# Optimization experiments

Measured on AMD Instinct MI355X. Metric: run time of the kernel, lower is better.

## Reference

```python
import jax, jax.numpy as jnp
import numpy as np

N, E = 100000, 400000
IN, HID, H, D = 165, 128, 8, 16  # per-head dim D = HID // H
NUM_CLASSES = 2


def layer_norm(x, g, b, eps=1e-5):
    m = jnp.mean(x, axis=-1, keepdims=True)
    v = jnp.var(x, axis=-1, keepdims=True)
    return (x - m) / jnp.sqrt(v + eps) * g + b


def transformer_conv(x, src, dst, Wq, bq, Wk, bk, Wv, bv, Ws, bs):
    # x: [N, HID]; src/dst: [E]
    n = x.shape[0]
    q = (x @ Wq + bq).reshape(n, H, D)
    k = (x @ Wk + bk).reshape(n, H, D)
    v = (x @ Wv + bv).reshape(n, H, D)
    # per-edge attention logits: [E, H]
    alpha = jnp.sum(q[dst] * k[src], axis=-1) / jnp.sqrt(jnp.float32(D))
    # segment softmax over incoming edges of each destination node
    amax = jax.ops.segment_max(alpha, dst, num_segments=n)          # [N, H]
    amax = jnp.where(jnp.isfinite(amax), amax, 0.0)
    ex = jnp.exp(alpha - amax[dst])                                  # [E, H]
    denom = jax.ops.segment_sum(ex, dst, num_segments=n)            # [N, H]
    a = ex / (denom[dst] + 1e-16)
    msg = v[src] * a[..., None]                                      # [E, H, D]
    out = jax.ops.segment_sum(msg, dst, num_segments=n)             # [N, H, D]
    out = out.reshape(n, H * D)
    # root skip connection (root_weight=True, beta=False in PyG defaults)
    return out + x @ Ws + bs


def setup_inputs() -> dict:
    key = jax.random.key(0)
    ks = jax.random.split(key, 24)
    rn = lambda k, s: (jax.random.normal(k, s, jnp.float32) * 0.05)
    inp = {
        "x": jax.random.normal(ks[0], (N, IN), jnp.float32),
        "edge_index": jax.random.randint(ks[1], (2, E), 0, N, jnp.int32),
        "W_in": rn(ks[2], (IN, HID)), "b_in": jnp.zeros((HID,), jnp.float32),
        # layer 1 TransformerConv
        "Wq1": rn(ks[3], (HID, HID)), "bq1": jnp.zeros((HID,), jnp.float32),
        "Wk1": rn(ks[4], (HID, HID)), "bk1": jnp.zeros((HID,), jnp.float32),
        "Wv1": rn(ks[5], (HID, HID)), "bv1": jnp.zeros((HID,), jnp.float32),
        "Ws1": rn(ks[6], (HID, HID)), "bs1": jnp.zeros((HID,), jnp.float32),
        "g1": jnp.ones((HID,), jnp.float32), "be1": jnp.zeros((HID,), jnp.float32),
        # layer 2 TransformerConv
        "Wq2": rn(ks[7], (HID, HID)), "bq2": jnp.zeros((HID,), jnp.float32),
        "Wk2": rn(ks[8], (HID, HID)), "bk2": jnp.zeros((HID,), jnp.float32),
        "Wv2": rn(ks[9], (HID, HID)), "bv2": jnp.zeros((HID,), jnp.float32),
        "Ws2": rn(ks[10], (HID, HID)), "bs2": jnp.zeros((HID,), jnp.float32),
        "g2": jnp.ones((HID,), jnp.float32), "be2": jnp.zeros((HID,), jnp.float32),
        # classifier MLP
        "Wc1": rn(ks[11], (HID, HID // 2)), "bc1": jnp.zeros((HID // 2,), jnp.float32),
        "Wc2": rn(ks[12], (HID // 2, NUM_CLASSES)), "bc2": jnp.zeros((NUM_CLASSES,), jnp.float32),
    }
    return inp


def reference(x, edge_index, W_in, b_in,
              Wq1, bq1, Wk1, bk1, Wv1, bv1, Ws1, bs1, g1, be1,
              Wq2, bq2, Wk2, bk2, Wv2, bv2, Ws2, bs2, g2, be2,
              Wc1, bc1, Wc2, bc2):
    src, dst = edge_index[0], edge_index[1]
    h = x @ W_in + b_in                                   # input projection
    h_new = transformer_conv(h, src, dst, Wq1, bq1, Wk1, bk1, Wv1, bv1, Ws1, bs1)
    h = layer_norm(h + h_new, g1, be1)                    # dropout = identity (eval)
    h_new = transformer_conv(h, src, dst, Wq2, bq2, Wk2, bk2, Wv2, bv2, Ws2, bs2)
    h = layer_norm(h + h_new, g2, be2)
    return jax.nn.relu(h @ Wc1 + bc1) @ Wc2 + bc2         # [N, num_classes]
```

## Files before the change

### kernel.cpp

```cpp
#include <hip/hip_runtime.h>
#include <hip/hip_bf16.h>

#define NN 100000
#define EE 400000
#define IN_DIM 165
#define KPAD 192
#define HID 128
#define C1 64
#define NC 2
#define SCANB 256
#define NBLK 391
#define NBD2 782

typedef const float* fpp;
typedef __hip_bfloat16 bf16;
typedef __attribute__((ext_vector_type(8))) short s16x8;
typedef __attribute__((ext_vector_type(4))) float f32x4;

__device__ __forceinline__ float bflo(unsigned u) { return __uint_as_float(u << 16); }
__device__ __forceinline__ float bfhi(unsigned u) { return __uint_as_float(u & 0xFFFF0000u); }
__device__ __forceinline__ float us2f(unsigned short u) { return __uint_as_float((unsigned)u << 16); }
__device__ __forceinline__ unsigned short bfbits(float f) {
    bf16 h = __float2bfloat16(f);
    return *reinterpret_cast<unsigned short*>(&h);
}

__global__ void k_cvt_weights(fpp W_in, fpp Wq1, fpp Wk1, fpp Wv1, fpp Ws1,
                              fpp Wq2, fpp Wk2, fpp Wv2, fpp Ws2, fpp Wc1,
                              fpp bq1, fpp bk1, fpp bv1, fpp bs1,
                              fpp bq2, fpp bk2, fpp bv2, fpp bs2,
                              unsigned short* __restrict__ winpack,
                              unsigned short* __restrict__ wpack,
                              unsigned short* __restrict__ wc1t,
                              float* __restrict__ bpack) {
    int idx = blockIdx.x * blockDim.x + threadIdx.x;
    if (idx < 24576) {
        int n = idx / KPAD, k = idx % KPAD;
        float v = (k < IN_DIM) ? W_in[k * HID + n] : 0.f;
        winpack[idx] = bfbits(v);
    } else if (idx < 155648) {
        int local = idx - 24576;
        int layer = local >> 16;
        int rest = local & 65535;
        int chunk = rest >> 14;
        int l14 = rest & 16383;
        int n = l14 >> 7, k = l14 & 127;
        const float* src;
        int col;
        if (chunk == 0) { src = layer ? Wq2 : Wq1; col = n; }
        else if (chunk == 3) { src = layer ? Ws2 : Ws1; col = n; }
        else {
            int a = ((chunk == 2) ? 16 : 0) + (n >> 3), e = n & 7;
            src = (e < 4) ? (layer ? Wk2 : Wk1) : (layer ? Wv2 : Wv1);
            col = 4 * a + (e & 3);
        }
        wpack[local] = bfbits(src[k * HID + col]);
    } else if (idx < 163840) {
        int local = idx - 155648;
        int n = local >> 7, k = local & 127;
        wc1t[local] = bfbits(Wc1[k * C1 + n]);
    } else if (idx < 164864) {
        int local = idx - 163840;
        int layer = local >> 9;
        int rest = local & 511;
        int chunk = rest >> 7, n = rest & 127;
        const float* src;
        int col;
        if (chunk == 0) { src = layer ? bq2 : bq1; col = n; }
        else if (chunk == 3) { src = layer ? bs2 : bs1; col = n; }
        else {
            int a = ((chunk == 2) ? 16 : 0) + (n >> 3), e = n & 7;
            src = (e < 4) ? (layer ? bk2 : bk1) : (layer ? bv2 : bv1);
            col = 4 * a + (e & 3);
        }
        bpack[local] = src[col];
    }
}

__global__ void k_cvt_x(fpp x, unsigned short* __restrict__ xb) {
    int i = blockIdx.x * blockDim.x + threadIdx.x;
    int row = i / 24, c = i % 24;
    s16x8 us;
#pragma unroll
    for (int j = 0; j < 8; j++) {
        int col = c * 8 + j;
        float v = (col < IN_DIM) ? x[(size_t)row * IN_DIM + col] : 0.f;
        us[j] = (short)bfbits(v);
    }
    *(s16x8*)(xb + (size_t)row * KPAD + c * 8) = us;
}

__global__ void k_hist(const int* __restrict__ dst, int* __restrict__ deg) {
    int e = blockIdx.x * blockDim.x + threadIdx.x;
    if (e < EE) atomicAdd(&deg[dst[e]], 1);
}
__global__ void k_scan1(const int* __restrict__ deg, int* __restrict__ pos,
                        int* __restrict__ bsum, int n) {
    __shared__ int tmp[SCANB];
    int t = threadIdx.x, i = blockIdx.x * SCANB + t;
    int v = (i < n) ? deg[i] : 0;
    tmp[t] = v; __syncthreads();
    for (int off = 1; off < SCANB; off <<= 1) {
        int x = (t >= off) ? tmp[t - off] : 0;
        __syncthreads();
        tmp[t] += x;
        __syncthreads();
    }
    if (i < n) pos[i] = tmp[t] - v;
    if (t == SCANB - 1) bsum[blockIdx.x] = tmp[t];
}
__global__ void k_scan2(int* __restrict__ bsum, int nb) {
    __shared__ int tmp[512];
    int t = threadIdx.x;
    int v = (t < nb) ? bsum[t] : 0;
    tmp[t] = v; __syncthreads();
    for (int off = 1; off < 512; off <<= 1) {
        int x = (t >= off) ? tmp[t - off] : 0;
        __syncthreads();
        tmp[t] += x;
        __syncthreads();
    }
    if (t < nb) bsum[t] = tmp[t] - v;
}
__global__ void k_scan3(int* __restrict__ pos, const int* __restrict__ bsum,
                        const int* __restrict__ deg, int2* __restrict__ csr2, int n) {
    int i = blockIdx.x * blockDim.x + threadIdx.x;
    if (i < n) {
        int s = pos[i] + bsum[blockIdx.x];
        pos[i] = s;
        csr2[i] = make_int2(s, deg[i]);
    }
}
__global__ void k_fill(const int* __restrict__ src, const int* __restrict__ dst,
                       int* __restrict__ pos, int* __restrict__ esrc) {
    int e = blockIdx.x * blockDim.x + threadIdx.x;
    if (e < EE) {
        int p = atomicAdd(&pos[dst[e]], 1);
        esrc[p] = src[e];
    }
}

__global__ __launch_bounds__(256) void k_dense_in(const unsigned short* __restrict__ xb,
                                                  const unsigned short* __restrict__ winpack,
                                                  fpp b_in, unsigned short* __restrict__ hb) {
    __shared__ unsigned short smem[18432];
    unsigned short* As = smem;
    unsigned short* Ws = smem + 9216;
    int row0 = blockIdx.x * 128;
    int t = threadIdx.x, lane = t & 63, w = t >> 6;
    int quad = lane >> 4, l16 = lane & 15;
    int m_off = (w >> 1) * 64, n_off = (w & 1) * 64;

    f32x4 acc[4][4];
    float bias_v[4];
#pragma unroll
    for (int ni = 0; ni < 4; ni++) bias_v[ni] = b_in[n_off + ni * 16 + l16];
#pragma unroll
    for (int mi = 0; mi < 4; mi++)
#pragma unroll
        for (int ni = 0; ni < 4; ni++)
            acc[mi][ni] = (f32x4){bias_v[ni], bias_v[ni], bias_v[ni], bias_v[ni]};

    for (int kc = 0; kc < 3; kc++) {
        __syncthreads();
        for (int i = 0; i < 4; i++) {
            int g = t + i * 256;
            int r = g >> 3, c = g & 7;
            int rg = min(row0 + r, NN - 1);
            *(s16x8*)(As + r * 72 + c * 8) =
                *(const s16x8*)(xb + (size_t)rg * KPAD + kc * 64 + c * 8);
            *(s16x8*)(Ws + r * 72 + c * 8) =
                *(const s16x8*)(winpack + r * KPAD + kc * 64 + c * 8);
        }
        __syncthreads();
#pragma unroll
        for (int ks = 0; ks < 2; ks++) {
            int k0 = ks * 32;
            s16x8 a[4], b[4];
#pragma unroll
            for (int mi = 0; mi < 4; mi++)
                a[mi] = *(const s16x8*)(As + (m_off + mi * 16 + l16) * 72 + k0 + quad * 8);
#pragma unroll
            for (int ni = 0; ni < 4; ni++)
                b[ni] = *(const s16x8*)(Ws + (n_off + ni * 16 + l16) * 72 + k0 + quad * 8);
#pragma unroll
            for (int mi = 0; mi < 4; mi++)
#pragma unroll
                for (int ni = 0; ni < 4; ni++)
                    acc[mi][ni] = __builtin_amdgcn_mfma_f32_16x16x32_bf16(
                        a[mi], b[ni], acc[mi][ni], 0, 0, 0);
        }
    }
    __syncthreads();
    unsigned short* Cs = smem;
#pragma unroll
    for (int mi = 0; mi < 4; mi++)
#pragma unroll
        for (int ni = 0; ni < 4; ni++)
#pragma unroll
            for (int r = 0; r < 4; r++)
                Cs[(m_off + mi * 16 + quad * 4 + r) * 136 + n_off + ni * 16 + l16] =
                    bfbits(acc[mi][ni][r]);
    __syncthreads();
    for (int i = 0; i < 8; i++) {
        int g = t + i * 256;
        int r = g >> 4, c = g & 15;
        if (row0 + r < NN)
            *(s16x8*)(hb + (size_t)(row0 + r) * HID + c * 8) =
                *(const s16x8*)(Cs + r * 136 + c * 8);
    }
}

__global__ __launch_bounds__(256) void k_dense4(const unsigned short* __restrict__ hb,
                                                const unsigned short* __restrict__ wpackL,
                                                const float* __restrict__ bpackL,
                                                bf16* __restrict__ qb, bf16* __restrict__ kvb,
                                                bf16* __restrict__ agg) {
    __shared__ unsigned short As[128 * 136];
    __shared__ unsigned short Ws[128 * 136];
    int row0 = blockIdx.x * 128;
    int t = threadIdx.x, lane = t & 63, w = t >> 6;
    int quad = lane >> 4, l16 = lane & 15;
    int m_off = (w >> 1) * 64, n_off = (w & 1) * 64;

    for (int i = 0; i < 8; i++) {
        int g = t + i * 256;
        int r = g >> 4, c = g & 15;
        int rg = min(row0 + r, NN - 1);
        *(s16x8*)(As + r * 136 + c * 8) = *(const s16x8*)(hb + (size_t)rg * HID + c * 8);
    }
    __syncthreads();

    s16x8 afr[4][4];
#pragma unroll
    for (int ks = 0; ks < 4; ks++)
#pragma unroll
        for (int mi = 0; mi < 4; mi++)
            afr[ks][mi] = *(const s16x8*)(As + (m_off + mi * 16 + l16) * 136 + ks * 32 + quad * 8);

    for (int nc = 0; nc < 4; nc++) {
        unsigned short* tp; int stride;
        if (nc == 0)      { tp = (unsigned short*)qb;        stride = 128; }
        else if (nc == 1) { tp = (unsigned short*)kvb;       stride = 256; }
        else if (nc == 2) { tp = (unsigned short*)kvb + 128; stride = 256; }
        else              { tp = (unsigned short*)agg;       stride = 128; }
        const float* bp = bpackL + nc * 128;

        __syncthreads();
        for (int i = 0; i < 8; i++) {
            int g = t + i * 256;
            int r = g >> 4, c = g & 15;
            *(s16x8*)(Ws + r * 136 + c * 8) =
                *(const s16x8*)(wpackL + nc * 16384 + r * HID + c * 8);
        }
        __syncthreads();

        f32x4 acc[4][4];
        float bias_v[4];
#pragma unroll
        for (int ni = 0; ni < 4; ni++) bias_v[ni] = bp[n_off + ni * 16 + l16];
#pragma unroll
        for (int mi = 0; mi < 4; mi++)
#pragma unroll
            for (int ni = 0; ni < 4; ni++)
                acc[mi][ni] = (f32x4){bias_v[ni], bias_v[ni], bias_v[ni], bias_v[ni]};

#pragma unroll
        for (int ks = 0; ks < 4; ks++) {
            s16x8 b[4];
#pragma unroll
            for (int ni = 0; ni < 4; ni++)
                b[ni] = *(const s16x8*)(Ws + (n_off + ni * 16 + l16) * 136 + ks * 32 + quad * 8);
#pragma unroll
            for (int mi = 0; mi < 4; mi++)
#pragma unroll
                for (int ni = 0; ni < 4; ni++)
                    acc[mi][ni] = __builtin_amdgcn_mfma_f32_16x16x32_bf16(
                        afr[ks][mi], b[ni], acc[mi][ni], 0, 0, 0);
        }
        __syncthreads();

        unsigned short* Cs = Ws;
#pragma unroll
        for (int mi = 0; mi < 4; mi++)
#pragma unroll
            for (int ni = 0; ni < 4; ni++)
#pragma unroll
                for (int r = 0; r < 4; r++)
                    Cs[(m_off + mi * 16 + quad * 4 + r) * 136 + n_off + ni * 16 + l16] =
                        bfbits(acc[mi][ni][r]);
        __syncthreads();
        if (nc == 3) {
            for (int i = 0; i < 8; i++) {
                int g = t + i * 256;
                int r = g >> 4, c = g & 15;
                if (row0 + r < NN) {
                    s16x8 cv = *(const s16x8*)(Cs + r * 136 + c * 8);
                    s16x8 hv = *(const s16x8*)(As + r * 136 + c * 8);
                    s16x8 ov;
#pragma unroll
                    for (int j = 0; j < 8; j++)
                        ov[j] = (short)bfbits(us2f((unsigned short)cv[j]) +
                                              us2f((unsigned short)hv[j]));
                    *(s16x8*)(tp + (size_t)(row0 + r) * stride + c * 8) = ov;
                }
            }
        } else {
            for (int i = 0; i < 8; i++) {
                int g = t + i * 256;
                int r = g >> 4, c = g & 15;
                if (row0 + r < NN)
                    *(s16x8*)(tp + (size_t)(row0 + r) * stride + c * 8) =
                        *(const s16x8*)(Cs + r * 136 + c * 8);
            }
        }
    }
}

__global__ void k_agg_ln(const bf16* __restrict__ qb, const bf16* __restrict__ kvb,
                         const int2* __restrict__ csr2, const int* __restrict__ esrc,
                         const bf16* __restrict__ agg, unsigned short* __restrict__ hb,
                         fpp g, fpp b) {
    int wv = (blockIdx.x * blockDim.x + threadIdx.x) >> 6;
    int lane = threadIdx.x & 63;
    int l32 = lane & 31;
    int d = wv * 2 + (lane >> 5);
    if (d >= NN) return;
    uint2 qu = ((const uint2*)(qb + (size_t)d * HID))[l32];
    float q0 = bflo(qu.x) * 0.25f, q1 = bfhi(qu.x) * 0.25f;
    float q2 = bflo(qu.y) * 0.25f, q3 = bfhi(qu.y) * 0.25f;
    int2 se = csr2[d];
    uint2 au = ((const uint2*)(agg + (size_t)d * HID))[l32];
    float4 gv = ((const float4*)g)[l32];
    float4 bv = ((const float4*)b)[l32];
    int start = se.x, cnt = se.y;

    int sj = (l32 < cnt) ? esrc[start + l32] : 0;

    uint4 kv[8];
    float tt[8];
    float m = -INFINITY;
#pragma unroll
    for (int j = 0; j < 8; j++) {
        int s = __shfl(sj, j, 32);
        if (j < cnt) kv[j] = ((const uint4*)(kvb + (size_t)s * 256))[l32];
        else kv[j] = (uint4){0u, 0u, 0u, 0u};
        float t = q0 * bflo(kv[j].x) + q1 * bfhi(kv[j].x) +
                  q2 * bflo(kv[j].y) + q3 * bfhi(kv[j].y);
        t += __shfl_xor(t, 1);
        t += __shfl_xor(t, 2);
        tt[j] = (j < cnt) ? t : -INFINITY;
        m = fmaxf(m, tt[j]);
    }
    if (cnt == 0) m = 0.f;
    float L = 0.f, o0 = 0.f, o1 = 0.f, o2 = 0.f, o3 = 0.f;
#pragma unroll
    for (int j = 0; j < 8; j++) {
        float p = __expf(tt[j] - m);
        L += p;
        o0 += p * bflo(kv[j].z);
        o1 += p * bfhi(kv[j].z);
        o2 += p * bflo(kv[j].w);
        o3 += p * bfhi(kv[j].w);
    }

    for (int j = 8; j < min(cnt, 32); j++) {
        int s = __shfl(sj, j, 32);
        uint4 kvt = ((const uint4*)(kvb + (size_t)s * 256))[l32];
        float t = q0 * bflo(kvt.x) + q1 * bfhi(kvt.x) + q2 * bflo(kvt.y) + q3 * bfhi(kvt.y);
        t += __shfl_xor(t, 1);
        t += __shfl_xor(t, 2);
        float nm = fmaxf(m, t);
        float corr = __expf(m - nm);
        float p = __expf(t - nm);
        L = L * corr + p;
        o0 = o0 * corr + p * bflo(kvt.z);
        o1 = o1 * corr + p * bfhi(kvt.z);
        o2 = o2 * corr + p * bflo(kvt.w);
        o3 = o3 * corr + p * bfhi(kvt.w);
        m = nm;
    }
    for (int base = 32; base < cnt; base += 32) {
        int nc = min(32, cnt - base);
        int sj2 = (l32 < nc) ? esrc[start + base + l32] : 0;
        for (int j = 0; j < nc; j++) {
            int s = __shfl(sj2, j, 32);
            uint4 kvt = ((const uint4*)(kvb + (size_t)s * 256))[l32];
            float t = q0 * bflo(kvt.x) + q1 * bfhi(kvt.x) + q2 * bflo(kvt.y) + q3 * bfhi(kvt.y);
            t += __shfl_xor(t, 1);
            t += __shfl_xor(t, 2);
            float nm = fmaxf(m, t);
            float corr = __expf(m - nm);
            float p = __expf(t - nm);
            L = L * corr + p;
            o0 = o0 * corr + p * bflo(kvt.z);
            o1 = o1 * corr + p * bfhi(kvt.z);
            o2 = o2 * corr + p * bflo(kvt.w);
            o3 = o3 * corr + p * bfhi(kvt.w);
            m = nm;
        }
    }

    float inv = 1.f / (L + 1e-16f);
    float v0 = bflo(au.x) + o0 * inv;
    float v1 = bfhi(au.x) + o1 * inv;
    float v2 = bflo(au.y) + o2 * inv;
    float v3 = bfhi(au.y) + o3 * inv;
    float s = v0 + v1 + v2 + v3;
    float s2 = v0 * v0 + v1 * v1 + v2 * v2 + v3 * v3;
    for (int off = 16; off; off >>= 1) {
        s += __shfl_xor(s, off);
        s2 += __shfl_xor(s2, off);
    }
    float mn = s * (1.f / HID);
    float var = s2 * (1.f / HID) - mn * mn;
    float invs = rsqrtf(var + 1e-5f);
    float ox = (v0 - mn) * invs * gv.x + bv.x;
    float oy = (v1 - mn) * invs * gv.y + bv.y;
    float oz = (v2 - mn) * invs * gv.z + bv.z;
    float ow = (v3 - mn) * invs * gv.w + bv.w;
    uint2 outw;
    outw.x = ((unsigned)bfbits(oy) << 16) | bfbits(ox);
    outw.y = ((unsigned)bfbits(ow) << 16) | bfbits(oz);
    ((uint2*)(hb + (size_t)d * HID))[l32] = outw;
}

__global__ __launch_bounds__(256) void k_classifier(const unsigned short* __restrict__ hb,
                                                    const unsigned short* __restrict__ wc1t,
                                                    fpp bc1, fpp Wc2, fpp bc2,
                                                    float* __restrict__ out) {
    __shared__ unsigned short As[128 * 136];
    __shared__ unsigned short Ws[64 * 136];
    int row0 = blockIdx.x * 128;
    int t = threadIdx.x, lane = t & 63, w = t >> 6;
    int quad = lane >> 4, l16 = lane & 15;
    int m_off = w * 32;

    for (int i = 0; i < 8; i++) {
        int g = t + i * 256;
        int r = g >> 4, c = g & 15;
        int rg = min(row0 + r, NN - 1);
        *(s16x8*)(As + r * 136 + c * 8) = *(const s16x8*)(hb + (size_t)rg * HID + c * 8);
    }
    for (int i = 0; i < 4; i++) {
        int g = t + i * 256;
        int r = g >> 4, c = g & 15;
        *(s16x8*)(Ws + r * 136 + c * 8) = *(const s16x8*)(wc1t + r * HID + c * 8);
    }
    __syncthreads();

    f32x4 acc[2][4];
    float bias_v[4];
#pragma unroll
    for (int ni = 0; ni < 4; ni++) bias_v[ni] = bc1[ni * 16 + l16];
#pragma unroll
    for (int mi = 0; mi < 2; mi++)
#pragma unroll
        for (int ni = 0; ni < 4; ni++)
            acc[mi][ni] = (f32x4){bias_v[ni], bias_v[ni], bias_v[ni], bias_v[ni]};

#pragma unroll
    for (int ks = 0; ks < 4; ks++) {
        s16x8 a[2], b[4];
#pragma unroll
        for (int mi = 0; mi < 2; mi++)
            a[mi] = *(const s16x8*)(As + (m_off + mi * 16 + l16) * 136 + ks * 32 + quad * 8);
#pragma unroll
        for (int ni = 0; ni < 4; ni++)
            b[ni] = *(const s16x8*)(Ws + (ni * 16 + l16) * 136 + ks * 32 + quad * 8);
#pragma unroll
        for (int mi = 0; mi < 2; mi++)
#pragma unroll
            for (int ni = 0; ni < 4; ni++)
                acc[mi][ni] = __builtin_amdgcn_mfma_f32_16x16x32_bf16(
                    a[mi], b[ni], acc[mi][ni], 0, 0, 0);
    }
    __syncthreads();
    float* Cs = (float*)As;
#pragma unroll
    for (int mi = 0; mi < 2; mi++)
#pragma unroll
        for (int ni = 0; ni < 4; ni++)
#pragma unroll
            for (int r = 0; r < 4; r++)
                Cs[(m_off + mi * 16 + quad * 4 + r) * 68 + ni * 16 + l16] =
                    fmaxf(acc[mi][ni][r], 0.f);
    __syncthreads();

    int row = t >> 1, half = t & 1;
    float p0 = 0.f, p1 = 0.f;
    for (int c = half * 32; c < half * 32 + 32; c++) {
        float v = Cs[row * 68 + c];
        p0 += v * Wc2[c * NC + 0];
        p1 += v * Wc2[c * NC + 1];
    }
    p0 += __shfl_xor(p0, 1, 64);
    p1 += __shfl_xor(p1, 1, 64);
    if (half == 0 && row0 + row < NN) {
        out[(size_t)(row0 + row) * NC + 0] = p0 + bc2[0];
        out[(size_t)(row0 + row) * NC + 1] = p1 + bc2[1];
    }
}

extern "C" void kernel_launch(void* const* d_in, const int* in_sizes, int n_in,
                              void* d_out, int out_size, void* d_ws, size_t ws_size,
                              hipStream_t stream) {
    fpp x = (fpp)d_in[0];
    const int* ei = (const int*)d_in[1];
    const int* src = ei;
    const int* dst = ei + EE;
    fpp W_in = (fpp)d_in[2];  fpp b_in = (fpp)d_in[3];
    fpp Wq1 = (fpp)d_in[4];   fpp bq1 = (fpp)d_in[5];
    fpp Wk1 = (fpp)d_in[6];   fpp bk1 = (fpp)d_in[7];
    fpp Wv1 = (fpp)d_in[8];   fpp bv1 = (fpp)d_in[9];
    fpp Ws1 = (fpp)d_in[10];  fpp bs1 = (fpp)d_in[11];
    fpp g1 = (fpp)d_in[12];   fpp be1 = (fpp)d_in[13];
    fpp Wq2 = (fpp)d_in[14];  fpp bq2 = (fpp)d_in[15];
    fpp Wk2 = (fpp)d_in[16];  fpp bk2 = (fpp)d_in[17];
    fpp Wv2 = (fpp)d_in[18];  fpp bv2 = (fpp)d_in[19];
    fpp Ws2 = (fpp)d_in[20];  fpp bs2 = (fpp)d_in[21];
    fpp g2 = (fpp)d_in[22];   fpp be2 = (fpp)d_in[23];
    fpp Wc1 = (fpp)d_in[24];  fpp bc1 = (fpp)d_in[25];
    fpp Wc2 = (fpp)d_in[26];  fpp bc2 = (fpp)d_in[27];
    float* out = (float*)d_out;

    char* p = (char*)d_ws;
    unsigned short* hb = (unsigned short*)p;  p += (size_t)NN * HID * 2;
    bf16* agg = (bf16*)p;            p += (size_t)NN * HID * 2;
    bf16* qb = (bf16*)p;             p += (size_t)NN * HID * 2;
    bf16* kvb = (bf16*)p;            p += (size_t)NN * 256 * 2;
    int* deg = (int*)p;              p += (size_t)NN * 4;
    int* pos = (int*)p;              p += (size_t)NN * 4;
    int2* csr2 = (int2*)p;           p += (size_t)NN * 8;
    int* esrc = (int*)p;             p += (size_t)EE * 4;
    int* bsum = (int*)p;             p += 512 * 4;
    unsigned short* winpack = (unsigned short*)p;  p += 24576 * 2;
    unsigned short* wpack = (unsigned short*)p;    p += 131072 * 2;
    unsigned short* wc1t = (unsigned short*)p;     p += 8192 * 2;
    float* bpack = (float*)p;                      p += 1024 * 4;
    unsigned short* xb = (unsigned short*)qb;

    const int nE = (EE + 255) / 256;

    k_cvt_weights<<<644, 256, 0, stream>>>(W_in, Wq1, Wk1, Wv1, Ws1,
                                           Wq2, Wk2, Wv2, Ws2, Wc1,
                                           bq1, bk1, bv1, bs1, bq2, bk2, bv2, bs2,
                                           winpack, wpack, wc1t, bpack);
    k_cvt_x<<<9375, 256, 0, stream>>>(x, xb);

    hipMemsetAsync(deg, 0, (size_t)NN * 4, stream);
    k_hist<<<nE, 256, 0, stream>>>(dst, deg);
    k_scan1<<<NBLK, SCANB, 0, stream>>>(deg, pos, bsum, NN);
    k_scan2<<<1, 512, 0, stream>>>(bsum, NBLK);
    k_scan3<<<NBLK, SCANB, 0, stream>>>(pos, bsum, deg, csr2, NN);
    k_fill<<<nE, 256, 0, stream>>>(src, dst, pos, esrc);

    k_dense_in<<<NBD2, 256, 0, stream>>>(xb, winpack, b_in, hb);

    for (int layer = 0; layer < 2; layer++) {
        fpp g = layer ? g2 : g1, be = layer ? be2 : be1;
        const unsigned short* wpackL = wpack + (size_t)layer * 65536;
        const float* bpackL = bpack + (size_t)layer * 512;

        k_dense4<<<NBD2, 256, 0, stream>>>(hb, wpackL, bpackL, qb, kvb, agg);
        k_agg_ln<<<12500, 256, 0, stream>>>(qb, kvb, csr2, esrc, agg, hb, g, be);
    }

    k_classifier<<<NBD2, 256, 0, stream>>>(hb, wc1t, bc1, Wc2, bc2, out);
}
```

Measured before the change: 406.0 us.

## Fuse histogram into weight prep, convert x inline, shrink aggregation prefetch

Merges the degree histogram into the weight-conversion kernel as extra blocks, which saves a launch. Removes the separate x-to-bf16 conversion kernel: the input projection now reads fp32 x directly and converts it while staging into shared memory, so the intermediate bf16 buffer is no longer written and re-read. Also shrinks the unrolled prefetch in the attention aggregation from 8 to 4 neighbours, which lowers register pressure. The cost is that edges beyond the fourth go through the serial online-softmax path, and the dense-in kernel now does uncoalesced fp32 loads with bounds checks.

```diff
diff --git a/kernel.cpp b/kernel.cpp
--- a/kernel.cpp
+++ b/kernel.cpp
@@ -11,6 +11,7 @@
 #define SCANB 256
 #define NBLK 391
 #define NBD2 782
+#define HBLK 1563
 
 typedef const float* fpp;
 typedef __hip_bfloat16 bf16;
@@ -25,15 +26,21 @@
     return *reinterpret_cast<unsigned short*>(&h);
 }
 
-__global__ void k_cvt_weights(fpp W_in, fpp Wq1, fpp Wk1, fpp Wv1, fpp Ws1,
-                              fpp Wq2, fpp Wk2, fpp Wv2, fpp Ws2, fpp Wc1,
-                              fpp bq1, fpp bk1, fpp bv1, fpp bs1,
-                              fpp bq2, fpp bk2, fpp bv2, fpp bs2,
-                              unsigned short* __restrict__ winpack,
-                              unsigned short* __restrict__ wpack,
-                              unsigned short* __restrict__ wc1t,
-                              float* __restrict__ bpack) {
-    int idx = blockIdx.x * blockDim.x + threadIdx.x;
+__global__ void k_prep(const int* __restrict__ dst, int* __restrict__ deg,
+                       fpp W_in, fpp Wq1, fpp Wk1, fpp Wv1, fpp Ws1,
+                       fpp Wq2, fpp Wk2, fpp Wv2, fpp Ws2, fpp Wc1,
+                       fpp bq1, fpp bk1, fpp bv1, fpp bs1,
+                       fpp bq2, fpp bk2, fpp bv2, fpp bs2,
+                       unsigned short* __restrict__ winpack,
+                       unsigned short* __restrict__ wpack,
+                       unsigned short* __restrict__ wc1t,
+                       float* __restrict__ bpack) {
+    if (blockIdx.x < HBLK) {
+        int e = blockIdx.x * 256 + threadIdx.x;
+        if (e < EE) atomicAdd(&deg[dst[e]], 1);
+        return;
+    }
+    int idx = (blockIdx.x - HBLK) * 256 + threadIdx.x;
     if (idx < 24576) {
         int n = idx / KPAD, k = idx % KPAD;
         float v = (k < IN_DIM) ? W_in[k * HID + n] : 0.f;
@@ -77,23 +84,6 @@
     }
 }
 
-__global__ void k_cvt_x(fpp x, unsigned short* __restrict__ xb) {
-    int i = blockIdx.x * blockDim.x + threadIdx.x;
-    int row = i / 24, c = i % 24;
-    s16x8 us;
-#pragma unroll
-    for (int j = 0; j < 8; j++) {
-        int col = c * 8 + j;
-        float v = (col < IN_DIM) ? x[(size_t)row * IN_DIM + col] : 0.f;
-        us[j] = (short)bfbits(v);
-    }
-    *(s16x8*)(xb + (size_t)row * KPAD + c * 8) = us;
-}
-
-__global__ void k_hist(const int* __restrict__ dst, int* __restrict__ deg) {
-    int e = blockIdx.x * blockDim.x + threadIdx.x;
-    if (e < EE) atomicAdd(&deg[dst[e]], 1);
-}
 __global__ void k_scan1(const int* __restrict__ deg, int* __restrict__ pos,
                         int* __restrict__ bsum, int n) {
     __shared__ int tmp[SCANB];
@@ -140,7 +130,7 @@
     }
 }
 
-__global__ __launch_bounds__(256) void k_dense_in(const unsigned short* __restrict__ xb,
+__global__ __launch_bounds__(256) void k_dense_in(const float* __restrict__ x,
                                                   const unsigned short* __restrict__ winpack,
                                                   fpp b_in, unsigned short* __restrict__ hb) {
     __shared__ unsigned short smem[18432];
@@ -167,10 +157,16 @@
             int g = t + i * 256;
             int r = g >> 3, c = g & 7;
             int rg = min(row0 + r, NN - 1);
-            *(s16x8*)(As + r * 72 + c * 8) =
-                *(const s16x8*)(xb + (size_t)rg * KPAD + kc * 64 + c * 8);
-            *(s16x8*)(Ws + r * 72 + c * 8) =
-                *(const s16x8*)(winpack + r * KPAD + kc * 64 + c * 8);
+            int col0 = kc * 64 + c * 8;
+            s16x8 us;
+#pragma unroll
+            for (int j = 0; j < 8; j++) {
+                int col = col0 + j;
+                float v = (col < IN_DIM) ? x[(size_t)rg * IN_DIM + col] : 0.f;
+                us[j] = (short)bfbits(v);
+            }
+            *(s16x8*)(As + r * 72 + c * 8) = us;
+            *(s16x8*)(Ws + r * 72 + c * 8) = *(const s16x8*)(winpack + r * KPAD + col0);
         }
         __syncthreads();
 #pragma unroll
@@ -337,11 +333,11 @@
 
     int sj = (l32 < cnt) ? esrc[start + l32] : 0;
 
-    uint4 kv[8];
-    float tt[8];
+    uint4 kv[4];
+    float tt[4];
     float m = -INFINITY;
 #pragma unroll
-    for (int j = 0; j < 8; j++) {
+    for (int j = 0; j < 4; j++) {
         int s = __shfl(sj, j, 32);
         if (j < cnt) kv[j] = ((const uint4*)(kvb + (size_t)s * 256))[l32];
         else kv[j] = (uint4){0u, 0u, 0u, 0u};
@@ -355,7 +351,7 @@
     if (cnt == 0) m = 0.f;
     float L = 0.f, o0 = 0.f, o1 = 0.f, o2 = 0.f, o3 = 0.f;
 #pragma unroll
-    for (int j = 0; j < 8; j++) {
+    for (int j = 0; j < 4; j++) {
         float p = __expf(tt[j] - m);
         L += p;
         o0 += p * bflo(kv[j].z);
@@ -364,7 +360,7 @@
         o3 += p * bfhi(kv[j].w);
     }
 
-    for (int j = 8; j < min(cnt, 32); j++) {
+    for (int j = 4; j < min(cnt, 32); j++) {
         int s = __shfl(sj, j, 32);
         uint4 kvt = ((const uint4*)(kvb + (size_t)s * 256))[l32];
         float t = q0 * bflo(kvt.x) + q1 * bfhi(kvt.x) + q2 * bflo(kvt.y) + q3 * bfhi(kvt.y);
@@ -538,24 +534,21 @@
     unsigned short* wpack = (unsigned short*)p;    p += 131072 * 2;
     unsigned short* wc1t = (unsigned short*)p;     p += 8192 * 2;
     float* bpack = (float*)p;                      p += 1024 * 4;
-    unsigned short* xb = (unsigned short*)qb;
 
     const int nE = (EE + 255) / 256;
 
-    k_cvt_weights<<<644, 256, 0, stream>>>(W_in, Wq1, Wk1, Wv1, Ws1,
+    hipMemsetAsync(deg, 0, (size_t)NN * 4, stream);
+    k_prep<<<HBLK + 644, 256, 0, stream>>>(dst, deg,
+                                           W_in, Wq1, Wk1, Wv1, Ws1,
                                            Wq2, Wk2, Wv2, Ws2, Wc1,
                                            bq1, bk1, bv1, bs1, bq2, bk2, bv2, bs2,
                                            winpack, wpack, wc1t, bpack);
-    k_cvt_x<<<9375, 256, 0, stream>>>(x, xb);
-
-    hipMemsetAsync(deg, 0, (size_t)NN * 4, stream);
-    k_hist<<<nE, 256, 0, stream>>>(dst, deg);
     k_scan1<<<NBLK, SCANB, 0, stream>>>(deg, pos, bsum, NN);
     k_scan2<<<1, 512, 0, stream>>>(bsum, NBLK);
     k_scan3<<<NBLK, SCANB, 0, stream>>>(pos, bsum, deg, csr2, NN);
     k_fill<<<nE, 256, 0, stream>>>(src, dst, pos, esrc);
 
-    k_dense_in<<<NBD2, 256, 0, stream>>>(xb, winpack, b_in, hb);
+    k_dense_in<<<NBD2, 256, 0, stream>>>(x, winpack, b_in, hb);
 
     for (int layer = 0; layer < 2; layer++) {
         fpp g = layer ? g2 : g1, be = layer ? be2 : be1;
```

New measurement: 386.0 us. -4.9%, faster.
